# Optimization experiments

Measured on AMD Instinct MI355X. Metric: run time of the kernel, lower is better.

The kernel has to match this reference:

```python
import jax, jax.numpy as jnp
import numpy as np

B, L, DIM, HEADS = 2, 2048, 1536, 12
HD = DIM // HEADS  # 128
C = HD // 2        # 64 rotary pairs
EPS = 1e-6


def setup_inputs() -> dict:
    key = jax.random.key(0)
    ks = jax.random.split(key, 8)
    x = jax.random.normal(ks[0], (B, L, DIM), jnp.float32)
    # ragged grids: sample0 fills L, sample1 has 2*24*32 = 1536 valid tokens
    grid_sizes = jnp.array([[2, 32, 32], [2, 24, 32]], dtype=jnp.int32)
    seq_lens = jnp.array([2048, 1536], dtype=jnp.int32)
    # rope freqs table [1024, C] (cos/sin of pos * inv_freq)
    pos = jnp.arange(1024, dtype=jnp.float32)[:, None]
    inv = 1.0 / (10000.0 ** (jnp.arange(C, dtype=jnp.float32) / C))
    ang = pos * inv
    freqs_cos, freqs_sin = jnp.cos(ang), jnp.sin(ang)
    init = lambda k: jax.random.normal(k, (DIM, DIM), jnp.float32) / np.sqrt(DIM)
    return dict(
        x=x, seq_lens=seq_lens, grid_sizes=grid_sizes,
        freqs_cos=freqs_cos, freqs_sin=freqs_sin,
        Wq=init(ks[1]), bq=jnp.zeros((DIM,), jnp.float32),
        Wk=init(ks[2]), bk=jnp.zeros((DIM,), jnp.float32),
        Wv=init(ks[3]), bv=jnp.zeros((DIM,), jnp.float32),
        Wo=init(ks[4]), bo=jnp.zeros((DIM,), jnp.float32),
        gq=jnp.ones((DIM,), jnp.float32), gk=jnp.ones((DIM,), jnp.float32),
    )


def _rope_one(xb, grid, cos, sin):
    # xb: [L, n, d]; grid: (f, h, w); cos/sin: [1024, C]
    f, h, w = grid[0], grid[1], grid[2]
    c = cos.shape[1]
    c2 = c // 3
    c1 = c - 2 * c2  # freqs split [c1, c2, c2] over axes (f, h, w)
    p = jnp.arange(xb.shape[0])
    hw = h * w
    valid = p < f * hw
    fi = jnp.where(valid, p // hw, 0)
    hi = jnp.where(valid, (p // w) % h, 0)
    wi = jnp.where(valid, p % w, 0)
    cos_p = jnp.concatenate([cos[fi, :c1], cos[hi, c1:c1 + c2], cos[wi, c1 + c2:]], axis=-1)
    sin_p = jnp.concatenate([sin[fi, :c1], sin[hi, c1:c1 + c2], sin[wi, c1 + c2:]], axis=-1)
    # positions beyond seq_len pass through unrotated (identity rotation)
    cos_p = jnp.where(valid[:, None], cos_p, 1.0)[:, None, :]  # [L,1,C]
    sin_p = jnp.where(valid[:, None], sin_p, 0.0)[:, None, :]
    xr, xi = xb[..., 0::2], xb[..., 1::2]
    out_r = xr * cos_p - xi * sin_p
    out_i = xr * sin_p + xi * cos_p
    return jnp.stack([out_r, out_i], axis=-1).reshape(xb.shape)


_rope_apply = jax.vmap(_rope_one, in_axes=(0, 0, None, None))


def _rms(t, g):
    t32 = t.astype(jnp.float32)
    return (t32 * jax.lax.rsqrt(jnp.mean(t32 * t32, axis=-1, keepdims=True) + EPS) * g).astype(t.dtype)


def reference(x, seq_lens, grid_sizes, freqs_cos, freqs_sin,
              Wq, bq, Wk, bk, Wv, bv, Wo, bo, gq, gk):
    b, s = x.shape[:2]
    n, d = HEADS, HD
    q = _rms(x @ Wq + bq, gq).reshape(b, s, n, d)
    k = _rms(x @ Wk + bk, gk).reshape(b, s, n, d)
    v = (x @ Wv + bv).reshape(b, s, n, d)
    q = _rope_apply(q, grid_sizes, freqs_cos, freqs_sin)
    k = _rope_apply(k, grid_sizes, freqs_cos, freqs_sin)
    scale = 1.0 / np.sqrt(d).astype(np.float32)
    scores = jnp.einsum('bqnd,bknd->bnqk', q, k) * scale
    kmask = jnp.arange(s)[None, :] < seq_lens[:, None]  # [b, s] key validity
    scores = jnp.where(kmask[:, None, None, :], scores, jnp.float32(-1e9))
    attn = jax.nn.softmax(scores, axis=-1)
    out = jnp.einsum('bnqk,bknd->bqnd', attn, v).reshape(b, s, n * d)
    return out @ Wo + bo
```

## Files before the change

### kernel.cpp

```cpp
#include <hip/hip_runtime.h>
#include <hip/hip_bf16.h>

#define DIM   1536
#define HEADS 12
#define HD    128
#define LSEQ  2048
#define NB    2
#define NTOK  (NB*LSEQ)

using f32x4 = __attribute__((ext_vector_type(4))) float;
using s16x8 = __attribute__((ext_vector_type(8))) short;
using u16x4 = __attribute__((ext_vector_type(4))) unsigned short;

__device__ __forceinline__ unsigned short f2bf(float f) {
  unsigned int u = __builtin_bit_cast(unsigned int, f);
  u += 0x7fffu + ((u >> 16) & 1u);
  return (unsigned short)(u >> 16);
}
__device__ __forceinline__ float bf2f(unsigned short u) {
  return __builtin_bit_cast(float, (unsigned int)u << 16);
}
__device__ __forceinline__ void gload_lds16(const void* g, void* l) {
  __builtin_amdgcn_global_load_lds(
      (__attribute__((address_space(1))) void*)const_cast<void*>(g),
      (__attribute__((address_space(3))) void*)l,
      16, 0, 0);
}

__global__ __launch_bounds__(256) void cvt_x(const float* __restrict__ x,
                                             unsigned short* __restrict__ xb, int n) {
  int i = (blockIdx.x * 256 + threadIdx.x) * 4;
  int stride = gridDim.x * 256 * 4;
  for (; i < n; i += stride) {
    f32x4 v = *(const f32x4*)(x + i);
    u16x4 o;
    o[0] = f2bf(v[0]); o[1] = f2bf(v[1]); o[2] = f2bf(v[2]); o[3] = f2bf(v[3]);
    *(u16x4*)(xb + i) = o;
  }
}

__global__ __launch_bounds__(256) void wtrans(const float* W0, const float* W1,
                                              const float* W2, const float* W3,
                                              unsigned short* __restrict__ Wt) {
  const float* W = blockIdx.z == 0 ? W0 : blockIdx.z == 1 ? W1 : blockIdx.z == 2 ? W2 : W3;
  unsigned short* out = Wt + (size_t)blockIdx.z * DIM * DIM;
  const int n0 = blockIdx.x * 64, k0 = blockIdx.y * 64;
  __shared__ unsigned short t[64][68];
  const int tid = threadIdx.x;
#pragma unroll
  for (int i = 0; i < 16; i++) {
    int idx = tid + i * 256;
    int r = idx >> 6, c = idx & 63;
    t[r][c] = f2bf(W[(size_t)(k0 + r) * DIM + n0 + c]);
  }
  __syncthreads();
#pragma unroll
  for (int i = 0; i < 16; i++) {
    int idx = tid + i * 256;
    int r = idx >> 6, c = idx & 63;
    out[(size_t)(n0 + r) * DIM + k0 + c] = t[c][r];
  }
}

__global__ __launch_bounds__(256) void gemm_bt(
    const unsigned short* __restrict__ A, const unsigned short* __restrict__ Bt,
    void* __restrict__ Cv,
    const float* __restrict__ b0, const float* __restrict__ b1, const float* __restrict__ b2,
    int M, int N, int K, int biasMode, int outBf16) {
  __shared__ __align__(16) unsigned short As[128 * 64];
  __shared__ __align__(16) unsigned short Bs[128 * 64];
  const int tid = threadIdx.x;
  const int lane = tid & 63, w = tid >> 6;
  const int wr = w >> 1, wc = w & 1;
  const int l15 = lane & 15, g4 = lane >> 4;
  const int nwg = gridDim.x * gridDim.y;
  const int bidf = blockIdx.y * gridDim.x + blockIdx.x;
  const int cpx = nwg >> 3;
  const int sw = (bidf & 7) * cpx + (bidf >> 3);
  const int m0 = (sw / gridDim.x) * 128, n0 = (sw % gridDim.x) * 128;

  f32x4 acc[4][4];
#pragma unroll
  for (int i = 0; i < 4; i++)
#pragma unroll
    for (int j = 0; j < 4; j++) acc[i][j] = (f32x4){0.f, 0.f, 0.f, 0.f};

  for (int kt = 0; kt < K; kt += 64) {
    __syncthreads();
#pragma unroll
    for (int i = 0; i < 4; i++) {
      int c = tid + i * 256;
      int row = c >> 3, g = c & 7;
      int gs = g ^ (row & 7);
      gload_lds16(A + (size_t)(m0 + row) * K + kt + gs * 8, As + c * 8);
    }
#pragma unroll
    for (int i = 0; i < 4; i++) {
      int c = tid + i * 256;
      int row = c >> 3, g = c & 7;
      int gs = g ^ (row & 7);
      gload_lds16(Bt + (size_t)(n0 + row) * K + kt + gs * 8, Bs + c * 8);
    }
    __syncthreads();
#pragma unroll
    for (int kk = 0; kk < 2; kk++) {
      s16x8 af[4], bfr[4];
#pragma unroll
      for (int m = 0; m < 4; m++) {
        int row = wr * 64 + m * 16 + l15;
        int off = row * 128 + ((kk * 64 + g4 * 16) ^ ((row & 7) << 4));
        af[m] = *(const s16x8*)((const char*)As + off);
      }
#pragma unroll
      for (int n = 0; n < 4; n++) {
        int row = wc * 64 + n * 16 + l15;
        int off = row * 128 + ((kk * 64 + g4 * 16) ^ ((row & 7) << 4));
        bfr[n] = *(const s16x8*)((const char*)Bs + off);
      }
#pragma unroll
      for (int m = 0; m < 4; m++)
#pragma unroll
        for (int n = 0; n < 4; n++)
          acc[m][n] = __builtin_amdgcn_mfma_f32_16x16x32_bf16(af[m], bfr[n], acc[m][n], 0, 0, 0);
    }
  }
#pragma unroll
  for (int m = 0; m < 4; m++)
#pragma unroll
    for (int n = 0; n < 4; n++)
#pragma unroll
      for (int r = 0; r < 4; r++) {
        int grow = m0 + wr * 64 + m * 16 + g4 * 4 + r;
        int gcol = n0 + wc * 64 + n * 16 + l15;
        float bias = (biasMode == 1)
                         ? b0[gcol]
                         : (gcol < 1536 ? b0[gcol]
                                        : (gcol < 3072 ? b1[gcol - 1536] : b2[gcol - 3072]));
        float val = acc[m][n][r] + bias;
        if (outBf16) ((unsigned short*)Cv)[(size_t)grow * N + gcol] = f2bf(val);
        else         ((float*)Cv)[(size_t)grow * N + gcol] = val;
      }
}

__global__ __launch_bounds__(256) void rmsrope(
    const unsigned short* __restrict__ qkvb,
    const float* __restrict__ gq, const float* __restrict__ gk,
    const int* __restrict__ grid_sizes,
    const float* __restrict__ fcos, const float* __restrict__ fsin,
    unsigned short* __restrict__ qb, unsigned short* __restrict__ kb) {
  const int t = blockIdx.x;
  const int b = t >> 11, l = t & 2047;
  const int tid = threadIdx.x;
  __shared__ float qrow[1536], krow[1536];
  __shared__ float red[8];
  const unsigned short* rq = qkvb + (size_t)t * 4608;
  const unsigned short* rk = rq + 1536;
  float sq = 0.f, sk = 0.f;
  if (tid < 192) {
    s16x8 vq = *(const s16x8*)(rq + tid * 8);
    s16x8 vk = *(const s16x8*)(rk + tid * 8);
#pragma unroll
    for (int j = 0; j < 8; j++) {
      float a = bf2f((unsigned short)vq[j]); qrow[tid * 8 + j] = a; sq += a * a;
      float c = bf2f((unsigned short)vk[j]); krow[tid * 8 + j] = c; sk += c * c;
    }
  }
  for (int o = 32; o; o >>= 1) { sq += __shfl_down(sq, o); sk += __shfl_down(sk, o); }
  if ((tid & 63) == 0) { red[tid >> 6] = sq; red[4 + (tid >> 6)] = sk; }
  __syncthreads();
  const float rsq = rsqrtf((red[0] + red[1] + red[2] + red[3]) * (1.f / 1536.f) + 1e-6f);
  const float rsk = rsqrtf((red[4] + red[5] + red[6] + red[7]) * (1.f / 1536.f) + 1e-6f);
  const float QS = 0.08838834764831845f;
  const int fg = grid_sizes[b * 3 + 0], hg = grid_sizes[b * 3 + 1], wg = grid_sizes[b * 3 + 2];
  const int hw = hg * wg;
  const bool valid = l < fg * hw;
  const int fi = valid ? l / hw : 0;
  const int hi = valid ? (l / wg) % hg : 0;
  const int wi = valid ? l % wg : 0;
  const size_t obase = (((size_t)b * HEADS) * LSEQ + l) * HD;
  for (int i = tid; i < HEADS * 64; i += 256) {
    int hd = i >> 6, j = i & 63;
    float c, s;
    if (valid) {
      int idx = j < 22 ? fi : (j < 43 ? hi : wi);
      c = fcos[idx * 64 + j]; s = fsin[idx * 64 + j];
    } else { c = 1.f; s = 0.f; }
    int col = hd * 128 + 2 * j;
    size_t o = obase + (size_t)hd * LSEQ * HD + 2 * j;
    float xr = qrow[col] * rsq * gq[col];
    float xi = qrow[col + 1] * rsq * gq[col + 1];
    float q0 = (xr * c - xi * s) * QS, q1 = (xr * s + xi * c) * QS;
    *(unsigned int*)(qb + o) = (unsigned int)f2bf(q0) | ((unsigned int)f2bf(q1) << 16);
    xr = krow[col] * rsk * gk[col];
    xi = krow[col + 1] * rsk * gk[col + 1];
    *(unsigned int*)(kb + o) =
        (unsigned int)f2bf(xr * c - xi * s) | ((unsigned int)f2bf(xr * s + xi * c) << 16);
  }
}

__global__ __launch_bounds__(256) void vtrans(const unsigned short* __restrict__ qkvb,
                                              unsigned short* __restrict__ vt) {
  const int lt = blockIdx.x, h = blockIdx.y, b = blockIdx.z;
  const int l0 = lt * 64;
  __shared__ unsigned short tile[64][130];
  const int tid = threadIdx.x;
#pragma unroll
  for (int i = 0; i < 4; i++) {
    int idx = tid + i * 256;
    int tk = idx >> 4, dc = (idx & 15) * 8;
    s16x8 v = *(const s16x8*)(qkvb + (size_t)(b * 2048 + l0 + tk) * 4608 + 3072 + h * 128 + dc);
#pragma unroll
    for (int j = 0; j < 8; j++) tile[tk][dc + j] = (unsigned short)v[j];
  }
  __syncthreads();
  const size_t ob = (((size_t)b * HEADS + h) * HD) * LSEQ + l0;
#pragma unroll
  for (int i = 0; i < 4; i++) {
    int idx = tid + i * 256;
    int d = idx >> 3, ck = (idx & 7) * 8;
    s16x8 o;
#pragma unroll
    for (int j = 0; j < 8; j++) o[j] = (short)tile[ck + j][d];
    *(s16x8*)(vt + ob + (size_t)d * LSEQ + ck) = o;
  }
}

__global__ __launch_bounds__(256) void flash(
    const unsigned short* __restrict__ qb, const unsigned short* __restrict__ kb,
    const unsigned short* __restrict__ vt, const int* __restrict__ seq_lens,
    unsigned short* __restrict__ ob) {
  const int qt = blockIdx.x, h = blockIdx.y, b = blockIdx.z;
  const int tid = threadIdx.x, lane = tid & 63, w = tid >> 6;
  const int l15 = lane & 15, g4 = lane >> 4;
  __shared__ __align__(16) unsigned short Ks[2][64 * 128];
  __shared__ __align__(16) unsigned short Vs[2][128 * 64];
  __shared__ __align__(16) unsigned short Pl[4][16 * 64];
  const size_t bh = (size_t)b * HEADS + h;
  const int q0 = qt * 64 + w * 16;
  s16x8 qf[4];
  {
    const unsigned short* qp = qb + (bh * LSEQ + q0 + l15) * HD;
#pragma unroll
    for (int c = 0; c < 4; c++) qf[c] = *(const s16x8*)(qp + c * 32 + g4 * 8);
  }
  const int ntile = seq_lens[b] >> 6;
  asm volatile("s_waitcnt vmcnt(0)" ::: "memory");

  union { unsigned short u[8]; s16x8 v; } ones_;
#pragma unroll
  for (int j = 0; j < 8; j++) ones_.u[j] = 0x3F80;

  f32x4 acc[9];
#pragma unroll
  for (int i = 0; i < 9; i++) acc[i] = (f32x4){0.f, 0.f, 0.f, 0.f};
  float mrow[4] = {-1e30f, -1e30f, -1e30f, -1e30f};
  char* pw = (char*)&Pl[w][0];

#define STAGE_K(T, BUF)                                                              \
  _Pragma("unroll") for (int i = 0; i < 4; i++) {                                    \
    int c = tid + i * 256, row = c >> 4, seg = c & 15, ss = seg ^ (row & 7);         \
    gload_lds16(kb + (bh * LSEQ + (T) * 64 + row) * HD + ss * 8, &Ks[BUF][0] + c * 8); \
  }
#define STAGE_V(T, BUF)                                                              \
  _Pragma("unroll") for (int i = 0; i < 4; i++) {                                    \
    int c = tid + i * 256, row = c >> 3, seg = c & 7, ss = seg ^ (row & 7);          \
    gload_lds16(vt + (bh * HD + row) * LSEQ + (T) * 64 + ss * 8, &Vs[BUF][0] + c * 8); \
  }

  STAGE_K(0, 0); STAGE_V(0, 0);
  STAGE_K(1, 1); STAGE_V(1, 1);

  for (int kt = 0; kt < ntile; kt++) {
    const int cur = kt & 1;
    asm volatile("s_waitcnt vmcnt(16)" ::: "memory");
    __builtin_amdgcn_s_barrier();
    __builtin_amdgcn_sched_barrier(0);
    f32x4 sv[4];
    __builtin_amdgcn_s_setprio(1);
#pragma unroll
    for (int n = 0; n < 4; n++) {
      f32x4 a = (f32x4){0.f, 0.f, 0.f, 0.f};
      int key = n * 16 + l15;
#pragma unroll
      for (int c = 0; c < 4; c++) {
        int off = key * 256 + ((c * 64 + g4 * 16) ^ ((key & 7) << 4));
        s16x8 kf = *(const s16x8*)((const char*)&Ks[cur][0] + off);
        a = __builtin_amdgcn_mfma_f32_16x16x32_bf16(qf[c], kf, a, 0, 0, 0);
      }
      sv[n] = a;
    }
    __builtin_amdgcn_s_setprio(0);
    float alpha_[4];
    bool anyGrow = false;
#pragma unroll
    for (int r = 0; r < 4; r++) {
      float v0 = sv[0][r], v1 = sv[1][r], v2 = sv[2][r], v3 = sv[3][r];
      float mx = fmaxf(fmaxf(v0, v1), fmaxf(v2, v3));
      unsigned long long vote = __ballot(mx > mrow[r] + 8.0f);
      bool grpGrow = ((vote >> (g4 * 16)) & 0xFFFFull) != 0;
      float mnew = mrow[r];
      float alpha = 1.f;
      if (grpGrow) {
#pragma unroll
        for (int o = 8; o; o >>= 1) mx = fmaxf(mx, __shfl_xor(mx, o));
        mnew = fmaxf(mrow[r], mx);
        alpha = __expf(mrow[r] - mnew);
      }
      float p0 = __expf(v0 - mnew), p1 = __expf(v1 - mnew);
      float p2 = __expf(v2 - mnew), p3 = __expf(v3 - mnew);
      mrow[r] = mnew; alpha_[r] = alpha; anyGrow |= grpGrow;
      int q = g4 * 4 + r;
      int swz = (q & 7) << 4;
      *(unsigned short*)(pw + q * 128 + ((2 * (0 * 16 + l15)) ^ swz)) = f2bf(p0);
      *(unsigned short*)(pw + q * 128 + ((2 * (1 * 16 + l15)) ^ swz)) = f2bf(p1);
      *(unsigned short*)(pw + q * 128 + ((2 * (2 * 16 + l15)) ^ swz)) = f2bf(p2);
      *(unsigned short*)(pw + q * 128 + ((2 * (3 * 16 + l15)) ^ swz)) = f2bf(p3);
    }
    if (__any((int)anyGrow)) {
#pragma unroll
      for (int dn = 0; dn < 9; dn++)
#pragma unroll
        for (int r = 0; r < 4; r++) acc[dn][r] *= alpha_[r];
    }
    s16x8 pa[2];
#pragma unroll
    for (int kk = 0; kk < 2; kk++) {
      int off = l15 * 128 + ((kk * 64 + g4 * 16) ^ ((l15 & 7) << 4));
      pa[kk] = *(const s16x8*)(pw + off);
    }
    __builtin_amdgcn_s_setprio(1);
#pragma unroll
    for (int dn = 0; dn < 8; dn++) {
      int d = dn * 16 + l15;
      int off0 = d * 128 + ((g4 * 16) ^ ((d & 7) << 4));
      int off1 = d * 128 + ((64 + g4 * 16) ^ ((d & 7) << 4));
      s16x8 vf0 = *(const s16x8*)((const char*)&Vs[cur][0] + off0);
      s16x8 vf1 = *(const s16x8*)((const char*)&Vs[cur][0] + off1);
      acc[dn] = __builtin_amdgcn_mfma_f32_16x16x32_bf16(pa[0], vf0, acc[dn], 0, 0, 0);
      acc[dn] = __builtin_amdgcn_mfma_f32_16x16x32_bf16(pa[1], vf1, acc[dn], 0, 0, 0);
    }
    acc[8] = __builtin_amdgcn_mfma_f32_16x16x32_bf16(pa[0], ones_.v, acc[8], 0, 0, 0);
    acc[8] = __builtin_amdgcn_mfma_f32_16x16x32_bf16(pa[1], ones_.v, acc[8], 0, 0, 0);
    __builtin_amdgcn_s_setprio(0);
    __builtin_amdgcn_s_barrier();
    __builtin_amdgcn_sched_barrier(0);
    if (kt + 2 < ntile) {
      STAGE_K(kt + 2, cur); STAGE_V(kt + 2, cur);
    } else if (kt < ntile - 1) {
      STAGE_K(kt, cur); STAGE_V(kt, cur);
    }
  }
  asm volatile("s_waitcnt vmcnt(0)" ::: "memory");
#undef STAGE_K
#undef STAGE_V
  float inv[4];
#pragma unroll
  for (int r = 0; r < 4; r++) inv[r] = 1.f / acc[8][r];
#pragma unroll
  for (int dn = 0; dn < 8; dn++)
#pragma unroll
    for (int r = 0; r < 4; r++) {
      int tok = b * LSEQ + qt * 64 + w * 16 + g4 * 4 + r;
      int col = h * HD + dn * 16 + l15;
      ob[(size_t)tok * DIM + col] = f2bf(acc[dn][r] * inv[r]);
    }
}

extern "C" void kernel_launch(void* const* d_in, const int* in_sizes, int n_in,
                              void* d_out, int out_size, void* d_ws, size_t ws_size,
                              hipStream_t stream) {
  const float* x    = (const float*)d_in[0];
  const int*   seq  = (const int*)d_in[1];
  const int*   grids= (const int*)d_in[2];
  const float* fcos = (const float*)d_in[3];
  const float* fsin = (const float*)d_in[4];
  const float* Wq   = (const float*)d_in[5];
  const float* bq   = (const float*)d_in[6];
  const float* Wk   = (const float*)d_in[7];
  const float* bk   = (const float*)d_in[8];
  const float* Wv   = (const float*)d_in[9];
  const float* bv   = (const float*)d_in[10];
  const float* Wo   = (const float*)d_in[11];
  const float* bo   = (const float*)d_in[12];
  const float* gq   = (const float*)d_in[13];
  const float* gk   = (const float*)d_in[14];

  char* ws = (char*)d_ws;
  unsigned short* xb   = (unsigned short*)(ws);
  unsigned short* Wt   = (unsigned short*)(ws + 12582912);
  unsigned short* qkvb = (unsigned short*)(ws + 31457280);
  unsigned short* qbb  = (unsigned short*)(ws + 69206016);
  unsigned short* kbb  = (unsigned short*)(ws + 81788928);
  unsigned short* vt   = (unsigned short*)d_out;
  unsigned short* obb  = xb;
  float* out = (float*)d_out;

  cvt_x<<<1024, 256, 0, stream>>>(x, xb, NTOK * DIM);
  wtrans<<<dim3(24, 24, 4), 256, 0, stream>>>(Wq, Wk, Wv, Wo, Wt);
  gemm_bt<<<dim3(36, 32), 256, 0, stream>>>(xb, Wt, qkvb, bq, bk, bv, NTOK, 3 * DIM, DIM, 0, 1);
  rmsrope<<<NTOK, 256, 0, stream>>>(qkvb, gq, gk, grids, fcos, fsin, qbb, kbb);
  vtrans<<<dim3(32, 12, 2), 256, 0, stream>>>(qkvb, vt);
  flash<<<dim3(32, 12, 2), 256, 0, stream>>>(qbb, kbb, vt, seq, obb);
  gemm_bt<<<dim3(12, 32), 256, 0, stream>>>(obb, Wt + (size_t)3 * DIM * DIM, out,
                                            bo, bo, bo, NTOK, DIM, DIM, 1, 0);
}
```

Baseline: 248.6 us.

## Rewrite flash attention with 32x32 MFMA, transposed scores, register-resident P

Switches the attention kernel from 16x16x32 MFMAs to 32x32x16 MFMAs. It computes S^T = K·Q^T so each lane owns one query row, which lets row max and row sum use in-register reductions plus a single cross-half shuffle. The P tile is packed to bf16 and redistributed with v_permlane32_swap instead of a round trip through LDS. The row sum is kept in a scalar rather than an extra ones-MFMA. Each workgroup now covers 128 queries (half the grid), blocks are remapped across XCDs, and output stores are packed 64-bit; the cost is more accumulator registers per thread and fewer workgroups.

```diff
diff --git a/kernel.cpp b/kernel.cpp
--- a/kernel.cpp
+++ b/kernel.cpp
@@ -8,9 +8,10 @@
 #define NB    2
 #define NTOK  (NB*LSEQ)
 
-using f32x4 = __attribute__((ext_vector_type(4))) float;
-using s16x8 = __attribute__((ext_vector_type(8))) short;
-using u16x4 = __attribute__((ext_vector_type(4))) unsigned short;
+using f32x4  = __attribute__((ext_vector_type(4))) float;
+using f32x16 = __attribute__((ext_vector_type(16))) float;
+using s16x8  = __attribute__((ext_vector_type(8))) short;
+using u16x4  = __attribute__((ext_vector_type(4))) unsigned short;
 
 __device__ __forceinline__ unsigned short f2bf(float f) {
   unsigned int u = __builtin_bit_cast(unsigned int, f);
@@ -19,6 +20,16 @@
 }
 __device__ __forceinline__ float bf2f(unsigned short u) {
   return __builtin_bit_cast(float, (unsigned int)u << 16);
+}
+__device__ __forceinline__ unsigned pk2(float a, float b) {
+  return (unsigned)f2bf(a) | ((unsigned)f2bf(b) << 16);
+}
+__device__ __forceinline__ unsigned long long pack4bf(float a, float b, float c, float d) {
+  return (unsigned long long)f2bf(a) | ((unsigned long long)f2bf(b) << 16) |
+         ((unsigned long long)f2bf(c) << 32) | ((unsigned long long)f2bf(d) << 48);
+}
+__device__ __forceinline__ void plswap(unsigned &x, unsigned &y) {
+  asm volatile("v_permlane32_swap_b32 %0, %1" : "+v"(x), "+v"(y));
 }
 __device__ __forceinline__ void gload_lds16(const void* g, void* l) {
   __builtin_amdgcn_global_load_lds(
@@ -229,41 +240,42 @@
     const unsigned short* __restrict__ qb, const unsigned short* __restrict__ kb,
     const unsigned short* __restrict__ vt, const int* __restrict__ seq_lens,
     unsigned short* __restrict__ ob) {
-  const int qt = blockIdx.x, h = blockIdx.y, b = blockIdx.z;
+  const int orig = blockIdx.x + 16 * (blockIdx.y + 12 * blockIdx.z);
+  const int wg = (orig & 7) * 48 + (orig >> 3);
+  const int qt = wg & 15;
+  const int hb = wg >> 4;
+  const int hh = hb % 12, b = hb / 12;
   const int tid = threadIdx.x, lane = tid & 63, w = tid >> 6;
-  const int l15 = lane & 15, g4 = lane >> 4;
+  const int l31 = lane & 31, hi = lane >> 5;
   __shared__ __align__(16) unsigned short Ks[2][64 * 128];
   __shared__ __align__(16) unsigned short Vs[2][128 * 64];
-  __shared__ __align__(16) unsigned short Pl[4][16 * 64];
-  const size_t bh = (size_t)b * HEADS + h;
-  const int q0 = qt * 64 + w * 16;
-  s16x8 qf[4];
+  const size_t bh = (size_t)b * HEADS + hh;
+  const int q0 = qt * 128 + w * 32;
+
+  s16x8 qf[8];
   {
-    const unsigned short* qp = qb + (bh * LSEQ + q0 + l15) * HD;
-#pragma unroll
-    for (int c = 0; c < 4; c++) qf[c] = *(const s16x8*)(qp + c * 32 + g4 * 8);
+    const unsigned short* qp = qb + (bh * LSEQ + q0 + l31) * HD + hi * 8;
+#pragma unroll
+    for (int s = 0; s < 8; s++) qf[s] = *(const s16x8*)(qp + s * 16);
   }
   const int ntile = seq_lens[b] >> 6;
   asm volatile("s_waitcnt vmcnt(0)" ::: "memory");
 
-  union { unsigned short u[8]; s16x8 v; } ones_;
-#pragma unroll
-  for (int j = 0; j < 8; j++) ones_.u[j] = 0x3F80;
-
-  f32x4 acc[9];
-#pragma unroll
-  for (int i = 0; i < 9; i++) acc[i] = (f32x4){0.f, 0.f, 0.f, 0.f};
-  float mrow[4] = {-1e30f, -1e30f, -1e30f, -1e30f};
-  char* pw = (char*)&Pl[w][0];
-
-#define STAGE_K(T, BUF)                                                              \
-  _Pragma("unroll") for (int i = 0; i < 4; i++) {                                    \
-    int c = tid + i * 256, row = c >> 4, seg = c & 15, ss = seg ^ (row & 7);         \
+  f32x16 acc[4];
+#pragma unroll
+  for (int d = 0; d < 4; d++)
+#pragma unroll
+    for (int r = 0; r < 16; r++) acc[d][r] = 0.f;
+  float mrow = -1e30f, ls = 0.f;
+
+#define STAGE_K(T, BUF)                                                                \
+  _Pragma("unroll") for (int i = 0; i < 4; i++) {                                      \
+    int c = tid + i * 256, row = c >> 4, seg = c & 15, ss = seg ^ (row & 7);           \
     gload_lds16(kb + (bh * LSEQ + (T) * 64 + row) * HD + ss * 8, &Ks[BUF][0] + c * 8); \
   }
-#define STAGE_V(T, BUF)                                                              \
-  _Pragma("unroll") for (int i = 0; i < 4; i++) {                                    \
-    int c = tid + i * 256, row = c >> 3, seg = c & 7, ss = seg ^ (row & 7);          \
+#define STAGE_V(T, BUF)                                                                \
+  _Pragma("unroll") for (int i = 0; i < 4; i++) {                                      \
+    int c = tid + i * 256, row = c >> 3, seg = c & 7, ss = seg ^ (row & 7);            \
     gload_lds16(vt + (bh * HD + row) * LSEQ + (T) * 64 + ss * 8, &Vs[BUF][0] + c * 8); \
   }
 
@@ -272,75 +284,81 @@
 
   for (int kt = 0; kt < ntile; kt++) {
     const int cur = kt & 1;
-    asm volatile("s_waitcnt vmcnt(16)" ::: "memory");
+    asm volatile("s_waitcnt vmcnt(8)" ::: "memory");
     __builtin_amdgcn_s_barrier();
     __builtin_amdgcn_sched_barrier(0);
-    f32x4 sv[4];
+    f32x16 st0, st1;
+#pragma unroll
+    for (int r = 0; r < 16; r++) { st0[r] = 0.f; st1[r] = 0.f; }
+    const char* ksb = (const char*)&Ks[cur][0];
     __builtin_amdgcn_s_setprio(1);
 #pragma unroll
-    for (int n = 0; n < 4; n++) {
-      f32x4 a = (f32x4){0.f, 0.f, 0.f, 0.f};
-      int key = n * 16 + l15;
-#pragma unroll
-      for (int c = 0; c < 4; c++) {
-        int off = key * 256 + ((c * 64 + g4 * 16) ^ ((key & 7) << 4));
-        s16x8 kf = *(const s16x8*)((const char*)&Ks[cur][0] + off);
-        a = __builtin_amdgcn_mfma_f32_16x16x32_bf16(qf[c], kf, a, 0, 0, 0);
+    for (int s = 0; s < 8; s++) {
+      int g = 2 * s + hi;
+      int r0 = l31, r1 = 32 + l31;
+      s16x8 kf0 = *(const s16x8*)(ksb + r0 * 256 + ((g ^ (r0 & 7)) << 4));
+      s16x8 kf1 = *(const s16x8*)(ksb + r1 * 256 + ((g ^ (r1 & 7)) << 4));
+      st0 = __builtin_amdgcn_mfma_f32_32x32x16_bf16(kf0, qf[s], st0, 0, 0, 0);
+      st1 = __builtin_amdgcn_mfma_f32_32x32x16_bf16(kf1, qf[s], st1, 0, 0, 0);
+    }
+    __builtin_amdgcn_s_setprio(0);
+    f32x16 mt;
+#pragma unroll
+    for (int r = 0; r < 16; r++) mt[r] = fmaxf(st0[r], st1[r]);
+#pragma unroll
+    for (int off = 8; off; off >>= 1)
+#pragma unroll
+      for (int r = 0; r < off; r++) mt[r] = fmaxf(mt[r], mt[r + off]);
+    float mx = fmaxf(mt[0], __shfl_xor(mt[0], 32));
+    const bool grow = mx > mrow + 8.0f;
+    const float alpha = grow ? __expf(mrow - mx) : 1.f;
+    if (grow) mrow = mx;
+#pragma unroll
+    for (int r = 0; r < 16; r++) { st0[r] = __expf(st0[r] - mrow); st1[r] = __expf(st1[r] - mrow); }
+    f32x16 sm;
+#pragma unroll
+    for (int r = 0; r < 16; r++) sm[r] = st0[r] + st1[r];
+#pragma unroll
+    for (int off = 8; off; off >>= 1)
+#pragma unroll
+      for (int r = 0; r < off; r++) sm[r] += sm[r + off];
+    ls = ls * alpha + (sm[0] + __shfl_xor(sm[0], 32));
+    if (__any((int)grow)) {
+#pragma unroll
+      for (int d = 0; d < 4; d++)
+#pragma unroll
+        for (int r = 0; r < 16; r++) acc[d][r] *= alpha;
+    }
+    union U { unsigned u[4]; s16x8 v; } pa0, pa1, pa2, pa3;
+    {
+      unsigned c0 = pk2(st0[0], st0[1]),  c1 = pk2(st0[2], st0[3]);
+      unsigned c2 = pk2(st0[4], st0[5]),  c3 = pk2(st0[6], st0[7]);
+      unsigned c4 = pk2(st0[8], st0[9]),  c5 = pk2(st0[10], st0[11]);
+      unsigned c6 = pk2(st0[12], st0[13]), c7 = pk2(st0[14], st0[15]);
+      plswap(c0, c2); plswap(c1, c3); plswap(c4, c6); plswap(c5, c7);
+      pa0.u[0] = c0; pa0.u[1] = c1; pa0.u[2] = c2; pa0.u[3] = c3;
+      pa1.u[0] = c4; pa1.u[1] = c5; pa1.u[2] = c6; pa1.u[3] = c7;
+      unsigned d0 = pk2(st1[0], st1[1]),  d1 = pk2(st1[2], st1[3]);
+      unsigned d2 = pk2(st1[4], st1[5]),  d3 = pk2(st1[6], st1[7]);
+      unsigned d4 = pk2(st1[8], st1[9]),  d5 = pk2(st1[10], st1[11]);
+      unsigned d6 = pk2(st1[12], st1[13]), d7 = pk2(st1[14], st1[15]);
+      plswap(d0, d2); plswap(d1, d3); plswap(d4, d6); plswap(d5, d7);
+      pa2.u[0] = d0; pa2.u[1] = d1; pa2.u[2] = d2; pa2.u[3] = d3;
+      pa3.u[0] = d4; pa3.u[1] = d5; pa3.u[2] = d6; pa3.u[3] = d7;
+    }
+    const char* vsb = (const char*)&Vs[cur][0];
+    __builtin_amdgcn_s_setprio(1);
+#pragma unroll
+    for (int slot = 0; slot < 4; slot++) {
+      s16x8 pb = slot == 0 ? pa0.v : slot == 1 ? pa1.v : slot == 2 ? pa2.v : pa3.v;
+      int g = 2 * slot + hi;
+#pragma unroll
+      for (int d = 0; d < 4; d++) {
+        int row = d * 32 + l31;
+        s16x8 vf = *(const s16x8*)(vsb + row * 128 + ((g ^ (row & 7)) << 4));
+        acc[d] = __builtin_amdgcn_mfma_f32_32x32x16_bf16(vf, pb, acc[d], 0, 0, 0);
       }
-      sv[n] = a;
-    }
-    __builtin_amdgcn_s_setprio(0);
-    float alpha_[4];
-    bool anyGrow = false;
-#pragma unroll
-    for (int r = 0; r < 4; r++) {
-      float v0 = sv[0][r], v1 = sv[1][r], v2 = sv[2][r], v3 = sv[3][r];
-      float mx = fmaxf(fmaxf(v0, v1), fmaxf(v2, v3));
-      unsigned long long vote = __ballot(mx > mrow[r] + 8.0f);
-      bool grpGrow = ((vote >> (g4 * 16)) & 0xFFFFull) != 0;
-      float mnew = mrow[r];
-      float alpha = 1.f;
-      if (grpGrow) {
-#pragma unroll
-        for (int o = 8; o; o >>= 1) mx = fmaxf(mx, __shfl_xor(mx, o));
-        mnew = fmaxf(mrow[r], mx);
-        alpha = __expf(mrow[r] - mnew);
-      }
-      float p0 = __expf(v0 - mnew), p1 = __expf(v1 - mnew);
-      float p2 = __expf(v2 - mnew), p3 = __expf(v3 - mnew);
-      mrow[r] = mnew; alpha_[r] = alpha; anyGrow |= grpGrow;
-      int q = g4 * 4 + r;
-      int swz = (q & 7) << 4;
-      *(unsigned short*)(pw + q * 128 + ((2 * (0 * 16 + l15)) ^ swz)) = f2bf(p0);
-      *(unsigned short*)(pw + q * 128 + ((2 * (1 * 16 + l15)) ^ swz)) = f2bf(p1);
-      *(unsigned short*)(pw + q * 128 + ((2 * (2 * 16 + l15)) ^ swz)) = f2bf(p2);
-      *(unsigned short*)(pw + q * 128 + ((2 * (3 * 16 + l15)) ^ swz)) = f2bf(p3);
-    }
-    if (__any((int)anyGrow)) {
-#pragma unroll
-      for (int dn = 0; dn < 9; dn++)
-#pragma unroll
-        for (int r = 0; r < 4; r++) acc[dn][r] *= alpha_[r];
-    }
-    s16x8 pa[2];
-#pragma unroll
-    for (int kk = 0; kk < 2; kk++) {
-      int off = l15 * 128 + ((kk * 64 + g4 * 16) ^ ((l15 & 7) << 4));
-      pa[kk] = *(const s16x8*)(pw + off);
-    }
-    __builtin_amdgcn_s_setprio(1);
-#pragma unroll
-    for (int dn = 0; dn < 8; dn++) {
-      int d = dn * 16 + l15;
-      int off0 = d * 128 + ((g4 * 16) ^ ((d & 7) << 4));
-      int off1 = d * 128 + ((64 + g4 * 16) ^ ((d & 7) << 4));
-      s16x8 vf0 = *(const s16x8*)((const char*)&Vs[cur][0] + off0);
-      s16x8 vf1 = *(const s16x8*)((const char*)&Vs[cur][0] + off1);
-      acc[dn] = __builtin_amdgcn_mfma_f32_16x16x32_bf16(pa[0], vf0, acc[dn], 0, 0, 0);
-      acc[dn] = __builtin_amdgcn_mfma_f32_16x16x32_bf16(pa[1], vf1, acc[dn], 0, 0, 0);
-    }
-    acc[8] = __builtin_amdgcn_mfma_f32_16x16x32_bf16(pa[0], ones_.v, acc[8], 0, 0, 0);
-    acc[8] = __builtin_amdgcn_mfma_f32_16x16x32_bf16(pa[1], ones_.v, acc[8], 0, 0, 0);
+    }
     __builtin_amdgcn_s_setprio(0);
     __builtin_amdgcn_s_barrier();
     __builtin_amdgcn_sched_barrier(0);
@@ -353,16 +371,15 @@
   asm volatile("s_waitcnt vmcnt(0)" ::: "memory");
 #undef STAGE_K
 #undef STAGE_V
-  float inv[4];
-#pragma unroll
-  for (int r = 0; r < 4; r++) inv[r] = 1.f / acc[8][r];
-#pragma unroll
-  for (int dn = 0; dn < 8; dn++)
-#pragma unroll
-    for (int r = 0; r < 4; r++) {
-      int tok = b * LSEQ + qt * 64 + w * 16 + g4 * 4 + r;
-      int col = h * HD + dn * 16 + l15;
-      ob[(size_t)tok * DIM + col] = f2bf(acc[dn][r] * inv[r]);
+  const float invl = 1.f / ls;
+  unsigned short* op = ob + (size_t)(b * LSEQ + q0 + l31) * DIM + hh * HD + hi * 4;
+#pragma unroll
+  for (int d = 0; d < 4; d++)
+#pragma unroll
+    for (int j = 0; j < 4; j++) {
+      unsigned long long pk = pack4bf(acc[d][4 * j] * invl, acc[d][4 * j + 1] * invl,
+                                      acc[d][4 * j + 2] * invl, acc[d][4 * j + 3] * invl);
+      *(unsigned long long*)(op + d * 32 + 8 * j) = pk;
     }
 }
 
@@ -400,7 +417,7 @@
   gemm_bt<<<dim3(36, 32), 256, 0, stream>>>(xb, Wt, qkvb, bq, bk, bv, NTOK, 3 * DIM, DIM, 0, 1);
   rmsrope<<<NTOK, 256, 0, stream>>>(qkvb, gq, gk, grids, fcos, fsin, qbb, kbb);
   vtrans<<<dim3(32, 12, 2), 256, 0, stream>>>(qkvb, vt);
-  flash<<<dim3(32, 12, 2), 256, 0, stream>>>(qbb, kbb, vt, seq, obb);
+  flash<<<dim3(16, 12, 2), 256, 0, stream>>>(qbb, kbb, vt, seq, obb);
   gemm_bt<<<dim3(12, 32), 256, 0, stream>>>(obb, Wt + (size_t)3 * DIM * DIM, out,
                                             bo, bo, bo, NTOK, DIM, DIM, 1, 0);
 }
```

Result: slower. 278.1 us (+11.8%).
